# Performance work log

Hardware: AMD Instinct MI355X
Metric: run time of the kernel (lower is better)

## Reference

```python
import jax, jax.numpy as jnp
from jax import lax
import numpy as np

B, T, IN, H, OUT = 1024, 100, 64, 512, 64


def setup_inputs() -> dict:
    key = jax.random.key(0)
    ks = jax.random.split(key, 16)
    s_in = 1.0 / np.sqrt(IN)
    s_h = 1.0 / np.sqrt(H)
    inp = {
        'coeffs': jax.random.normal(ks[0], (B, T - 1, 4, IN), jnp.float32),
        'times': jnp.linspace(0.0, 1.0, T, dtype=jnp.float32),
        'dW': jax.random.normal(ks[1], (T - 1, B, H), jnp.float32),
        # initial_network: Linear(IN, H)
        'W_init': jax.random.normal(ks[2], (IN, H), jnp.float32) * s_in,
        'b_init': jnp.zeros((H,), jnp.float32),
        # drift MLP f: H -> H -> H
        'Wf1': jax.random.normal(ks[3], (H, H), jnp.float32) * s_h,
        'bf1': jnp.zeros((H,), jnp.float32),
        'Wf2': jax.random.normal(ks[4], (H, H), jnp.float32) * s_h,
        'bf2': jnp.zeros((H,), jnp.float32),
        # diffusion MLP g: H -> H -> H (tanh-bounded, diagonal noise)
        'Wg1': jax.random.normal(ks[5], (H, H), jnp.float32) * s_h,
        'bg1': jnp.zeros((H,), jnp.float32),
        'Wg2': jax.random.normal(ks[6], (H, H), jnp.float32) * s_h,
        'bg2': jnp.zeros((H,), jnp.float32),
        # readout: Tanh -> Linear(H,H) -> ReLU -> Linear(H,OUT)
        'Wl1': jax.random.normal(ks[7], (H, H), jnp.float32) * s_h,
        'bl1': jnp.zeros((H,), jnp.float32),
        'Wl2': jax.random.normal(ks[8], (H, OUT), jnp.float32) * s_h,
        'bl2': jnp.zeros((OUT,), jnp.float32),
    }
    return inp


def reference(coeffs, times, dW, W_init, b_init, Wf1, bf1, Wf2, bf2,
              Wg1, bg1, Wg2, bg2, Wl1, bl1, Wl2, bl2):
    # y0 = X.evaluate(times[0]) == constant coefficient of first spline segment
    x0 = coeffs[:, 0, 0, :]                      # [B, IN]
    y0 = x0 @ W_init + b_init                    # [B, H]

    def f(y):
        return jnp.tanh(y @ Wf1 + bf1) @ Wf2 + bf2

    def g(y):
        return jnp.tanh(jnp.tanh(y @ Wg1 + bg1) @ Wg2 + bg2)

    hs = times[1:] - times[:-1]                  # [T-1], equals dt on uniform grid

    def step(y, inp):
        h, dw = inp
        y_next = y + f(y) * h + g(y) * (jnp.sqrt(h) * dw)
        return y_next, y_next

    _, ys = lax.scan(step, y0, (hs, dW))         # ys: [T-1, B, H]
    z = jnp.concatenate([y0[None], ys], axis=0)  # [T, B, H]
    z = jnp.transpose(z, (1, 0, 2))              # [B, T, H]  (permute(1,0,2))

    # readout: Tanh -> Linear -> ReLU -> Linear
    out = jax.nn.relu(jnp.tanh(z) @ Wl1 + bl1) @ Wl2 + bl2  # [B, T, OUT]
    return out, z
```

## Files before the change

kernel.cpp:

```cpp
#include <hip/hip_runtime.h>
#include <hip/hip_bf16.h>
#include <math.h>

#define DEV __device__ __forceinline__

typedef __attribute__((ext_vector_type(8))) short short8;
typedef __attribute__((ext_vector_type(4))) float f32x4;
typedef __attribute__((ext_vector_type(4))) unsigned int u32x4;

static constexpr int Bsz  = 1024;
static constexpr int T    = 100;
static constexpr int TM1  = 99;
static constexpr int H    = 512;
static constexpr int OUTD = 64;
static constexpr int H2   = 1024;
static constexpr int BT   = Bsz * T;

DEV unsigned short f2bf(float f){
  unsigned int u = __float_as_uint(f);
  u += 0x7fffu + ((u >> 16) & 1u);
  return (unsigned short)(u >> 16);
}
DEV unsigned pack2(float lo, float hi){
  return (unsigned)f2bf(lo) | ((unsigned)f2bf(hi) << 16);
}
DEV float tanh_fast(float x){
  x = fminf(fmaxf(x, -15.f), 15.f);
  float e = __expf(2.f * x);
  return (e - 1.f) / (e + 1.f);
}

#define AISSUE_CC(dst, p) asm volatile("global_load_dwordx4 %0, %1, off sc0 sc1" : "=&v"(dst) : "v"(p) : "memory")
#define AISSUE_L2(dst, p) asm volatile("global_load_dwordx4 %0, %1, off sc0"     : "=&v"(dst) : "v"(p) : "memory")
#define PLOAD(dst, p)  asm volatile("global_load_dword %0, %1, off"          : "=&v"(dst) : "v"(p) : "memory")
#define SC_STORE(p, v) asm volatile("global_store_dword %0, %1, off sc0 sc1" :: "v"(p), "v"(v) : "memory")
#define VWAIT(n)       asm volatile("s_waitcnt vmcnt(" #n ")" ::: "memory"); __builtin_amdgcn_sched_barrier(0)

DEV void gbar(unsigned* cnt, unsigned target){
  __syncthreads();
  if (threadIdx.x == 0){
    __hip_atomic_fetch_add(cnt, 1u, __ATOMIC_RELAXED, __HIP_MEMORY_SCOPE_AGENT);
    while (__hip_atomic_load(cnt, __ATOMIC_RELAXED, __HIP_MEMORY_SCOPE_AGENT) < target)
      __builtin_amdgcn_s_sleep(1);
  }
  __syncthreads();
}

__global__ __launch_bounds__(256) void k_prep(const float* __restrict__ Wf1, const float* __restrict__ Wg1,
                                              const float* __restrict__ Wf2, const float* __restrict__ Wg2,
                                              const float* __restrict__ Wl1, const float* __restrict__ Wl2,
                                              unsigned short* __restrict__ W1T, unsigned short* __restrict__ W2T,
                                              unsigned short* __restrict__ Wl1F, unsigned short* __restrict__ Wl2F){
  __shared__ float tl[32][33];
  const float* src; unsigned short* dst; int N; int fmt;
  switch (blockIdx.z){
    case 0: src = Wf1; dst = W1T;             N = 512; fmt = 0; break;
    case 1: src = Wg1; dst = W1T + 512*512;   N = 512; fmt = 0; break;
    case 2: src = Wf2; dst = W2T;             N = 512; fmt = 0; break;
    case 3: src = Wg2; dst = W2T + 512*512;   N = 512; fmt = 0; break;
    case 4: src = Wl1; dst = Wl1F;            N = 512; fmt = 1; break;
    default: src = Wl2; dst = Wl2F;           N = 64;  fmt = 2; break;
  }
  int k0 = blockIdx.x*32, n0 = blockIdx.y*32;
  if (n0 >= N) return;
  int tx = threadIdx.x, ty = threadIdx.y;
  #pragma unroll
  for (int r = 0; r < 4; r++) tl[ty + r*8][tx] = src[(size_t)(k0 + ty + r*8) * N + n0 + tx];
  __syncthreads();
  if (fmt == 0){
    int kpos = k0 + ((tx & 15)*2 + (tx >> 4));
    #pragma unroll
    for (int r = 0; r < 4; r++) dst[(size_t)(n0 + ty + r*8) * 512 + kpos] = f2bf(tl[tx][ty + r*8]);
  } else {
    int k = k0 + tx;
    int Nc = (fmt == 1) ? 512 : 64;
    #pragma unroll
    for (int r = 0; r < 4; r++){
      int col = n0 + ty + r*8;
      size_t idx = (((size_t)(k >> 5)*Nc + col)*4 + ((k >> 3) & 3))*8 + (k & 7);
      dst[idx] = f2bf(tl[tx][ty + r*8]);
    }
  }
}

__global__ void k_zero(unsigned* __restrict__ cnts){
  cnts[threadIdx.x + blockIdx.x*256] = 0u;
}

#define KSX(K, W, LD) \
  VWAIT(W); \
  { short8 a_  = *(short8*)&ap[(K)&7]; \
    short8 b0_ = *(const short8*)(wbp + (K)*4096); \
    short8 b1_ = *(const short8*)(wbp + (K)*4096 + 1024); \
    p0 = __builtin_amdgcn_mfma_f32_16x16x32_bf16(a_, b0_, p0, 0,0,0); \
    p1 = __builtin_amdgcn_mfma_f32_16x16x32_bf16(a_, b1_, p1, 0,0,0); } \
  if ((K) < 8) { LD(ap[(K)&7], abp + (size_t)((K)+8)*65536); }

#define RUN16X(LD) \
  LD(ap[0], abp);          LD(ap[1], abp+65536); \
  LD(ap[2], abp+131072);   LD(ap[3], abp+196608); \
  LD(ap[4], abp+262144);   LD(ap[5], abp+327680); \
  LD(ap[6], abp+393216);   LD(ap[7], abp+458752); \
  KSX( 0,7,LD) KSX( 1,7,LD) KSX( 2,7,LD) KSX( 3,7,LD) \
  KSX( 4,7,LD) KSX( 5,7,LD) KSX( 6,7,LD) KSX( 7,7,LD) \
  KSX( 8,7,LD) KSX( 9,6,LD) KSX(10,5,LD) KSX(11,4,LD) \
  KSX(12,3,LD) KSX(13,2,LD) KSX(14,1,LD) KSX(15,0,LD)

template<int UNIQ>
__global__ __launch_bounds__(512, 1) void k_scan(
    const float* __restrict__ coeffs, const float* __restrict__ times,
    const float* __restrict__ dW,     const float* __restrict__ W_init,
    const float* __restrict__ b_init,
    const unsigned short* __restrict__ W1T, const unsigned short* __restrict__ W2T,
    const float* __restrict__ bf1, const float* __restrict__ bg1,
    const float* __restrict__ bf2, const float* __restrict__ bg2,
    unsigned short* __restrict__ ygk, unsigned short* __restrict__ uk,
    float* __restrict__ z, unsigned* __restrict__ cnts){
  __shared__ __align__(16) unsigned char W1s[65536];
  __shared__ __align__(16) unsigned char W2s[65536];
  __shared__ __align__(16) float cmb[64*68];
  __shared__ float tms[104];

  constexpr size_t YB = UNIQ ? (size_t)Bsz * H  * 2 : 0;
  constexpr size_t UB = UNIQ ? (size_t)Bsz * H2 * 2 : 0;

  const int bid = blockIdx.x, mt = bid & 15, ns = bid >> 4;
  const int m0 = mt*64, n1 = ns*64, n2 = ns*32;
  const int tid = threadIdx.x, lane = tid & 63, w = tid >> 6;
  const int fr = lane & 15, fq = lane >> 4;
  const int band = w & 3, isg = w >> 2;
  unsigned* cnt = cnts + mt*32;
  unsigned ep = 0;

  #pragma unroll
  for (int i = 0; i < 8; i++){
    int u = i*512 + tid;
    int fqi = u & 3, cl = (u >> 2) & 63, kc = u >> 8;
    *(uint4*)(W1s + (size_t)u*16) = *(const uint4*)(W1T + (size_t)(n1+cl)*512 + kc*32 + fqi*8);
    const unsigned short* s2 = (cl < 32) ? (W2T + (size_t)(n2+cl)*512)
                                         : (W2T + (size_t)262144 + (size_t)(n2+cl-32)*512);
    *(uint4*)(W2s + (size_t)u*16) = *(const uint4*)(s2 + kc*32 + fqi*8);
  }
  if (tid < 100) tms[tid] = times[tid];
  { int row = tid >> 3, c0 = (tid & 7)*8;
    const float* src = coeffs + (size_t)(m0+row)*(TM1*4*64) + c0;
    *(float4*)(&cmb[row*68 + c0])     = *(const float4*)src;
    *(float4*)(&cmb[row*68 + c0 + 4]) = *(const float4*)(src + 4);
  }
  __syncthreads();

  char* ygkb = (char*)ygk;
  char* ukb  = (char*)uk;
  const char* ab1 = ygkb + ((size_t)(m0 + band*16 + fr))*64 + fq*16;
  const char* ab2 = ukb + (size_t)isg*1048576 + ((size_t)(m0 + band*16 + fr))*64 + fq*16;
  char* up = ukb  + (size_t)(ns*2 + isg)*65536 + ((size_t)(m0 + band*16 + fq*4))*64 + fr*4;
  char* yp = ygkb + (size_t)ns*65536           + ((size_t)(m0 + band*16 + fq*4))*64 + fr*4;
  const unsigned char* wbp1 = W1s + isg*2048 + fr*64 + fq*16;
  const unsigned char* wbp2 = W2s + isg*2048 + fr*64 + fq*16;
  float* zp = z + ((size_t)(m0 + band*16 + fq*4))*T*512 + n2 + fr;

  const float* b1src = (ns < 8) ? bf1 : bg1;
  const int    b1off = n1 - ((ns < 8) ? 0 : 512) + isg*32 + fr;
  const float b1v0 = b1src[b1off], b1v1 = b1src[b1off + 16];
  const float* b2src = isg ? bg2 : bf2;
  const float b2v0 = b2src[n2 + fr], b2v1 = b2src[n2 + 16 + fr];

  float yv[2][4];
  if (isg){
    #pragma unroll
    for (int r = 0; r < 4; r++){
      int lrow = band*16 + fq*4 + r;
      float s0 = b_init[n2 + fr], s1 = b_init[n2 + 16 + fr];
      #pragma unroll 8
      for (int k = 0; k < 64; k++){
        float xv = cmb[lrow*68 + k];
        s0 += xv * W_init[(size_t)k*512 + n2 + fr];
        s1 += xv * W_init[(size_t)k*512 + n2 + 16 + fr];
      }
      yv[0][r] = s0; yv[1][r] = s1;
      SC_STORE(yp + r*64, pack2(s0, s1));
      zp[(size_t)r*T*512]      = s0;
      zp[(size_t)r*T*512 + 16] = s1;
    }
    VWAIT(8);
  }
  ++ep; gbar(cnt, ep*16);

  for (int t = 0; t < TM1; t++){
    float dv[8];
    {
      f32x4 p0 = {0.f,0.f,0.f,0.f}, p1 = {0.f,0.f,0.f,0.f};
      u32x4 ap[8];
      const char* abp = ab1 + (size_t)t*YB;
      const unsigned char* wbp = wbp1;
      if constexpr (UNIQ) { RUN16X(AISSUE_L2); } else { RUN16X(AISSUE_CC); }
      char* upt = up + (size_t)t*UB;
      #pragma unroll
      for (int r = 0; r < 4; r++)
        SC_STORE(upt + r*64, pack2(tanh_fast(p0[r] + b1v0), tanh_fast(p1[r] + b1v1)));
      if (isg){
        const char* dp = (const char*)dW + (((size_t)t*1024 + m0 + band*16 + fq*4)*512 + n2 + fr)*4;
        PLOAD(dv[0], dp + 0);      PLOAD(dv[1], dp + 64);
        PLOAD(dv[2], dp + 2048);   PLOAD(dv[3], dp + 2048+64);
        PLOAD(dv[4], dp + 4096);   PLOAD(dv[5], dp + 4096+64);
        PLOAD(dv[6], dp + 6144);   PLOAD(dv[7], dp + 6144+64);
        VWAIT(8);
      } else {
        VWAIT(0);
      }
    }
    ++ep; gbar(cnt, ep*16);

    {
      f32x4 p0 = {0.f,0.f,0.f,0.f}, p1 = {0.f,0.f,0.f,0.f};
      u32x4 ap[8];
      const char* abp = ab2 + (size_t)t*UB;
      const unsigned char* wbp = wbp2;
      if constexpr (UNIQ) { RUN16X(AISSUE_L2); } else { RUN16X(AISSUE_CC); }
      if (!isg){
        #pragma unroll
        for (int r = 0; r < 4; r++){
          int lrow = band*16 + fq*4 + r;
          cmb[lrow*68 + fr]      = p0[r] + b2v0;
          cmb[lrow*68 + 16 + fr] = p1[r] + b2v1;
        }
      }
      __syncthreads();
      if (isg){
        float h  = tms[t+1] - tms[t];
        float sq = sqrtf(h);
        char* ypt = yp + (size_t)(t+1)*YB;
        #pragma unroll
        for (int r = 0; r < 4; r++){
          int lrow = band*16 + fq*4 + r;
          float f0 = cmb[lrow*68 + fr],       f1 = cmb[lrow*68 + 16 + fr];
          float g0 = tanh_fast(p0[r] + b2v0), g1 = tanh_fast(p1[r] + b2v1);
          float y0n = yv[0][r] + f0*h + g0*(sq*dv[r*2]);
          float y1n = yv[1][r] + f1*h + g1*(sq*dv[r*2+1]);
          yv[0][r] = y0n; yv[1][r] = y1n;
          SC_STORE(ypt + r*64, pack2(y0n, y1n));
          zp[(size_t)r*T*512 + (size_t)(t+1)*512]      = y0n;
          zp[(size_t)r*T*512 + (size_t)(t+1)*512 + 16] = y1n;
        }
        VWAIT(8);
      }
    }
    if (t < TM1-1){ ++ep; gbar(cnt, ep*16); }
  }
}

__global__ __launch_bounds__(512, 1) void k_read(
    const float* __restrict__ z, const unsigned short* __restrict__ Wl1F,
    const float* __restrict__ bl1, const unsigned short* __restrict__ Wl2F,
    const float* __restrict__ bl2, float* __restrict__ out){
  __shared__ __align__(16) unsigned char zt[65536];
  __shared__ __align__(16) unsigned char relF[65536];
  const int tid = threadIdx.x, lane = tid & 63, w = tid >> 6;
  const int fr = lane & 15, fq = lane >> 4;
  const size_t rr0 = (size_t)blockIdx.x * 64;
  const int cw = w * 64;

  { int row = tid >> 3, c0 = (tid & 7) * 64;
    const float* zr = z + (rr0 + row) * 512 + c0;
    #pragma unroll
    for (int j = 0; j < 2; ++j){
      int kc = (c0 >> 5) + j;
      #pragma unroll
      for (int f = 0; f < 4; ++f){
        float4 v0 = *(const float4*)(zr + j*32 + f*8);
        float4 v1 = *(const float4*)(zr + j*32 + f*8 + 4);
        unsigned d0 = pack2(tanh_fast(v0.x), tanh_fast(v0.y));
        unsigned d1 = pack2(tanh_fast(v0.z), tanh_fast(v0.w));
        unsigned d2 = pack2(tanh_fast(v1.x), tanh_fast(v1.y));
        unsigned d3 = pack2(tanh_fast(v1.z), tanh_fast(v1.w));
        uint4 pk = {d0, d1, d2, d3};
        *(uint4*)(zt + (size_t)((kc*64 + row)*4 + f)*16) = pk;
      }
    }
  }
  __syncthreads();

  f32x4 acc[4][4];
  #pragma unroll
  for (int m = 0; m < 4; m++)
    #pragma unroll
    for (int c = 0; c < 4; c++) acc[m][c] = (f32x4){0.f,0.f,0.f,0.f};
  for (int kc = 0; kc < 16; ++kc){
    short8 a[4];
    #pragma unroll
    for (int m = 0; m < 4; m++)
      a[m] = *(const short8*)(zt + (size_t)((kc*64 + m*16 + fr)*4 + fq)*16);
    #pragma unroll
    for (int c = 0; c < 4; c++){
      short8 b = *(const short8*)(Wl1F + (((size_t)kc*512 + cw + c*16 + fr)*4 + fq)*8);
      #pragma unroll
      for (int m = 0; m < 4; m++)
        acc[m][c] = __builtin_amdgcn_mfma_f32_16x16x32_bf16(a[m], b, acc[m][c], 0, 0, 0);
    }
  }
  float bl1v[4];
  #pragma unroll
  for (int c = 0; c < 4; c++) bl1v[c] = bl1[cw + c*16 + fr];

  #pragma unroll
  for (int h = 0; h < 2; ++h){
    __syncthreads();
    if ((w >> 2) == h){
      float* stg = (float*)zt;
      int cb = cw - h*256;
      #pragma unroll
      for (int m = 0; m < 4; m++)
        #pragma unroll
        for (int c = 0; c < 4; c++)
          #pragma unroll
          for (int r = 0; r < 4; r++)
            stg[(m*16 + fq*4 + r)*256 + cb + c*16 + fr] = fmaxf(acc[m][c][r] + bl1v[c], 0.f);
    }
    __syncthreads();
    { int row = tid >> 3, c8 = (tid & 7) * 32;
      const float* stg = (const float*)zt;
      int kc = h*8 + (tid & 7);
      #pragma unroll
      for (int f = 0; f < 4; ++f){
        const float* p = stg + row*256 + c8 + f*8;
        unsigned d0 = pack2(p[0], p[1]);
        unsigned d1 = pack2(p[2], p[3]);
        unsigned d2 = pack2(p[4], p[5]);
        unsigned d3 = pack2(p[6], p[7]);
        uint4 pk = {d0, d1, d2, d3};
        *(uint4*)(relF + (size_t)((kc*64 + row)*4 + f)*16) = pk;
      }
    }
  }
  __syncthreads();

  f32x4 acc2[2];
  acc2[0] = (f32x4){0.f,0.f,0.f,0.f};
  acc2[1] = (f32x4){0.f,0.f,0.f,0.f};
  const int mt2 = w & 3, ocb = (w >> 2) * 32;
  for (int kc = 0; kc < 16; ++kc){
    short8 a = *(const short8*)(relF + (size_t)((kc*64 + mt2*16 + fr)*4 + fq)*16);
    #pragma unroll
    for (int j = 0; j < 2; j++){
      short8 b = *(const short8*)(Wl2F + (((size_t)(kc*64 + ocb + j*16 + fr))*4 + fq)*8);
      acc2[j] = __builtin_amdgcn_mfma_f32_16x16x32_bf16(a, b, acc2[j], 0, 0, 0);
    }
  }
  #pragma unroll
  for (int j = 0; j < 2; j++){
    #pragma unroll
    for (int r = 0; r < 4; r++){
      int row = mt2*16 + fq*4 + r;
      int oc  = ocb + j*16 + fr;
      out[(rr0 + row)*64 + oc] = acc2[j][r] + bl2[oc];
    }
  }
}

extern "C" void kernel_launch(void* const* d_in, const int* in_sizes, int n_in,
                              void* d_out, int out_size, void* d_ws, size_t ws_size,
                              hipStream_t stream){
  (void)in_sizes; (void)n_in; (void)out_size;
  const float* coeffs = (const float*)d_in[0];
  const float* times  = (const float*)d_in[1];
  const float* dW     = (const float*)d_in[2];
  const float* W_init = (const float*)d_in[3];
  const float* b_init = (const float*)d_in[4];
  const float* Wf1 = (const float*)d_in[5];
  const float* bf1 = (const float*)d_in[6];
  const float* Wf2 = (const float*)d_in[7];
  const float* bf2 = (const float*)d_in[8];
  const float* Wg1 = (const float*)d_in[9];
  const float* bg1 = (const float*)d_in[10];
  const float* Wg2 = (const float*)d_in[11];
  const float* bg2 = (const float*)d_in[12];
  const float* Wl1 = (const float*)d_in[13];
  const float* bl1 = (const float*)d_in[14];
  const float* Wl2 = (const float*)d_in[15];
  const float* bl2 = (const float*)d_in[16];

  float* out = (float*)d_out;
  float* z   = out + (size_t)Bsz * T * OUTD;

  const bool full = ws_size >= ((size_t)320 << 20);

  char* wsp = (char*)d_ws;
  auto carve = [&](size_t bytes) -> void* {
    void* p = (void*)wsp; wsp += (bytes + 255) & ~(size_t)255; return p;
  };
  unsigned short* W1T  = (unsigned short*)carve((size_t)H2 * H * 2);
  unsigned short* W2T  = (unsigned short*)carve((size_t)H2 * H * 2);
  unsigned short* Wl1F = (unsigned short*)carve((size_t)H * H * 2);
  unsigned short* Wl2F = (unsigned short*)carve((size_t)OUTD * H * 2);
  unsigned short* ygk  = (unsigned short*)carve(full ? (size_t)T   * Bsz * H  * 2
                                                     : (size_t)Bsz * H  * 2);
  unsigned short* uk   = (unsigned short*)carve(full ? (size_t)TM1 * Bsz * H2 * 2
                                                     : (size_t)Bsz * H2 * 2);
  unsigned*       cnts = (unsigned*)carve(1024 * sizeof(unsigned));

  k_zero<<<dim3(4), 256, 0, stream>>>(cnts);
  k_prep<<<dim3(16, 16, 6), dim3(32, 8), 0, stream>>>(Wf1, Wg1, Wf2, Wg2, Wl1, Wl2,
                                                      W1T, W2T, Wl1F, Wl2F);
  if (full)
    k_scan<1><<<dim3(256), 512, 0, stream>>>(coeffs, times, dW, W_init, b_init,
                                             W1T, W2T, bf1, bg1, bf2, bg2,
                                             ygk, uk, z, cnts);
  else
    k_scan<0><<<dim3(256), 512, 0, stream>>>(coeffs, times, dW, W_init, b_init,
                                             W1T, W2T, bf1, bg1, bf2, bg2,
                                             ygk, uk, z, cnts);
  k_read<<<dim3(BT / 64), 512, 0, stream>>>(z, Wl1F, bl1, Wl2F, bl2, out);
}
```

Baseline: 937.2 us.

## Split grid barrier, prefetch own y chunk across it, rotate K order, swizzle LDS

The grid barrier is split into arrive and wait halves. Between them each block issues the load for the first A chunk of the next y-GEMM, which is the slice that block wrote itself, so the barrier latency overlaps with a global load. In the first GEMM the K loop is rotated by the block's column index so different blocks start on different L2 lines. The weight tiles in LDS are XOR-swizzled to reduce bank conflicts. The risk is that the early prefetch relies on the block's own stores being visible before the wait completes.

```diff
diff --git a/kernel.cpp b/kernel.cpp
--- a/kernel.cpp
+++ b/kernel.cpp
@@ -36,10 +36,13 @@
 #define SC_STORE(p, v) asm volatile("global_store_dword %0, %1, off sc0 sc1" :: "v"(p), "v"(v) : "memory")
 #define VWAIT(n)       asm volatile("s_waitcnt vmcnt(" #n ")" ::: "memory"); __builtin_amdgcn_sched_barrier(0)
 
-DEV void gbar(unsigned* cnt, unsigned target){
-  __syncthreads();
+DEV void gbar_arrive(unsigned* cnt){
+  __syncthreads();
+  if (threadIdx.x == 0)
+    __hip_atomic_fetch_add(cnt, 1u, __ATOMIC_RELAXED, __HIP_MEMORY_SCOPE_AGENT);
+}
+DEV void gbar_wait(unsigned* cnt, unsigned target){
   if (threadIdx.x == 0){
-    __hip_atomic_fetch_add(cnt, 1u, __ATOMIC_RELAXED, __HIP_MEMORY_SCOPE_AGENT);
     while (__hip_atomic_load(cnt, __ATOMIC_RELAXED, __HIP_MEMORY_SCOPE_AGENT) < target)
       __builtin_amdgcn_s_sleep(1);
   }
@@ -90,8 +93,8 @@
 #define KSX(K, W, LD) \
   VWAIT(W); \
   { short8 a_  = *(short8*)&ap[(K)&7]; \
-    short8 b0_ = *(const short8*)(wbp + (K)*4096); \
-    short8 b1_ = *(const short8*)(wbp + (K)*4096 + 1024); \
+    short8 b0_ = *(const short8*)(wbp + (size_t)(K)*4096); \
+    short8 b1_ = *(const short8*)(wbp + (size_t)(K)*4096 + 1024); \
     p0 = __builtin_amdgcn_mfma_f32_16x16x32_bf16(a_, b0_, p0, 0,0,0); \
     p1 = __builtin_amdgcn_mfma_f32_16x16x32_bf16(a_, b1_, p1, 0,0,0); } \
   if ((K) < 8) { LD(ap[(K)&7], abp + (size_t)((K)+8)*65536); }
@@ -105,6 +108,29 @@
   KSX( 4,7,LD) KSX( 5,7,LD) KSX( 6,7,LD) KSX( 7,7,LD) \
   KSX( 8,7,LD) KSX( 9,6,LD) KSX(10,5,LD) KSX(11,4,LD) \
   KSX(12,3,LD) KSX(13,2,LD) KSX(14,1,LD) KSX(15,0,LD)
+
+#define C16(K) (((K) + rot) & 15)
+#define KSXR(K, W, LD) \
+  VWAIT(W); \
+  { short8 a_  = *(short8*)&ap[(K)&7]; \
+    short8 b0_ = *(const short8*)(wbp + (size_t)C16(K)*4096); \
+    short8 b1_ = *(const short8*)(wbp + (size_t)C16(K)*4096 + 1024); \
+    p0 = __builtin_amdgcn_mfma_f32_16x16x32_bf16(a_, b0_, p0, 0,0,0); \
+    p1 = __builtin_amdgcn_mfma_f32_16x16x32_bf16(a_, b1_, p1, 0,0,0); } \
+  if ((K) < 8) { LD(ap[(K)&7], abp + (size_t)C16((K)+8)*65536); }
+
+#define RUN16R(LD) \
+  LD(ap[1], abp + (size_t)C16(1)*65536); \
+  LD(ap[2], abp + (size_t)C16(2)*65536); \
+  LD(ap[3], abp + (size_t)C16(3)*65536); \
+  LD(ap[4], abp + (size_t)C16(4)*65536); \
+  LD(ap[5], abp + (size_t)C16(5)*65536); \
+  LD(ap[6], abp + (size_t)C16(6)*65536); \
+  LD(ap[7], abp + (size_t)C16(7)*65536); \
+  KSXR( 0,7,LD) KSXR( 1,7,LD) KSXR( 2,7,LD) KSXR( 3,7,LD) \
+  KSXR( 4,7,LD) KSXR( 5,7,LD) KSXR( 6,7,LD) KSXR( 7,7,LD) \
+  KSXR( 8,7,LD) KSXR( 9,6,LD) KSXR(10,5,LD) KSXR(11,4,LD) \
+  KSXR(12,3,LD) KSXR(13,2,LD) KSXR(14,1,LD) KSXR(15,0,LD)
 
 template<int UNIQ>
 __global__ __launch_bounds__(512, 1) void k_scan(
@@ -129,6 +155,7 @@
   const int tid = threadIdx.x, lane = tid & 63, w = tid >> 6;
   const int fr = lane & 15, fq = lane >> 4;
   const int band = w & 3, isg = w >> 2;
+  const int rot = ns;
   unsigned* cnt = cnts + mt*32;
   unsigned ep = 0;
 
@@ -136,10 +163,11 @@
   for (int i = 0; i < 8; i++){
     int u = i*512 + tid;
     int fqi = u & 3, cl = (u >> 2) & 63, kc = u >> 8;
-    *(uint4*)(W1s + (size_t)u*16) = *(const uint4*)(W1T + (size_t)(n1+cl)*512 + kc*32 + fqi*8);
+    size_t dstoff = (size_t)kc*4096 + (size_t)((cl*64 + fqi*16) ^ ((cl & 7) << 4));
+    *(uint4*)(W1s + dstoff) = *(const uint4*)(W1T + (size_t)(n1+cl)*512 + kc*32 + fqi*8);
     const unsigned short* s2 = (cl < 32) ? (W2T + (size_t)(n2+cl)*512)
                                          : (W2T + (size_t)262144 + (size_t)(n2+cl-32)*512);
-    *(uint4*)(W2s + (size_t)u*16) = *(const uint4*)(s2 + kc*32 + fqi*8);
+    *(uint4*)(W2s + dstoff) = *(const uint4*)(s2 + kc*32 + fqi*8);
   }
   if (tid < 100) tms[tid] = times[tid];
   { int row = tid >> 3, c0 = (tid & 7)*8;
@@ -155,8 +183,8 @@
   const char* ab2 = ukb + (size_t)isg*1048576 + ((size_t)(m0 + band*16 + fr))*64 + fq*16;
   char* up = ukb  + (size_t)(ns*2 + isg)*65536 + ((size_t)(m0 + band*16 + fq*4))*64 + fr*4;
   char* yp = ygkb + (size_t)ns*65536           + ((size_t)(m0 + band*16 + fq*4))*64 + fr*4;
-  const unsigned char* wbp1 = W1s + isg*2048 + fr*64 + fq*16;
-  const unsigned char* wbp2 = W2s + isg*2048 + fr*64 + fq*16;
+  const unsigned char* wbp1 = W1s + isg*2048 + (size_t)((fr*64 + fq*16) ^ ((fr & 7) << 4));
+  const unsigned char* wbp2 = W2s + isg*2048 + (size_t)((fr*64 + fq*16) ^ ((fr & 7) << 4));
   float* zp = z + ((size_t)(m0 + band*16 + fq*4))*T*512 + n2 + fr;
 
   const float* b1src = (ns < 8) ? bf1 : bg1;
@@ -164,6 +192,8 @@
   const float b1v0 = b1src[b1off], b1v1 = b1src[b1off + 16];
   const float* b2src = isg ? bg2 : bf2;
   const float b2v0 = b2src[n2 + fr], b2v1 = b2src[n2 + 16 + fr];
+
+  u32x4 ap[8];
 
   float yv[2][4];
   if (isg){
@@ -184,16 +214,18 @@
     }
     VWAIT(8);
   }
-  ++ep; gbar(cnt, ep*16);
+  ++ep; gbar_arrive(cnt);
+  if constexpr (UNIQ) { AISSUE_L2(ap[0], ab1 + (size_t)rot*65536); }
+  else                { AISSUE_CC(ap[0], ab1 + (size_t)rot*65536); }
+  gbar_wait(cnt, ep*16);
 
   for (int t = 0; t < TM1; t++){
     float dv[8];
     {
       f32x4 p0 = {0.f,0.f,0.f,0.f}, p1 = {0.f,0.f,0.f,0.f};
-      u32x4 ap[8];
       const char* abp = ab1 + (size_t)t*YB;
       const unsigned char* wbp = wbp1;
-      if constexpr (UNIQ) { RUN16X(AISSUE_L2); } else { RUN16X(AISSUE_CC); }
+      if constexpr (UNIQ) { RUN16R(AISSUE_L2); } else { RUN16R(AISSUE_CC); }
       char* upt = up + (size_t)t*UB;
       #pragma unroll
       for (int r = 0; r < 4; r++)
@@ -209,11 +241,10 @@
         VWAIT(0);
       }
     }
-    ++ep; gbar(cnt, ep*16);
+    ++ep; gbar_arrive(cnt); gbar_wait(cnt, ep*16);
 
     {
       f32x4 p0 = {0.f,0.f,0.f,0.f}, p1 = {0.f,0.f,0.f,0.f};
-      u32x4 ap[8];
       const char* abp = ab2 + (size_t)t*UB;
       const unsigned char* wbp = wbp2;
       if constexpr (UNIQ) { RUN16X(AISSUE_L2); } else { RUN16X(AISSUE_CC); }
@@ -245,7 +276,14 @@
         VWAIT(8);
       }
     }
-    if (t < TM1-1){ ++ep; gbar(cnt, ep*16); }
+    if (t < TM1-1){
+      ++ep; gbar_arrive(cnt);
+      { const char* pib = ab1 + (size_t)(t+1)*YB;
+        if constexpr (UNIQ) { AISSUE_L2(ap[0], pib + (size_t)rot*65536); }
+        else                { AISSUE_CC(ap[0], pib + (size_t)rot*65536); }
+      }
+      gbar_wait(cnt, ep*16);
+    }
   }
 }
 
```

Measured after the change: 930.9 us. Within noise of the previous version (-0.7%).

## Split K dimension across two wave groups in scan kernel with LDS reduction

Applied to the files above, without the earlier changes.

Doubles the scan kernel's block size to 1024 threads and splits each GEMM's K loop in half across two wave groups. The upper half writes its partial sums to shared memory, and the lower half adds them before applying tanh and the SDE update. The weight tiles in shared memory also get an XOR swizzle to reduce bank conflicts on the B-operand reads. The aim is to halve the serial MFMA chain per step on this latency-bound recurrent path, at the cost of extra __syncthreads and shared-memory traffic per step.

```diff
diff --git a/kernel.cpp b/kernel.cpp
--- a/kernel.cpp
+++ b/kernel.cpp
@@ -87,27 +87,24 @@
   cnts[threadIdx.x + blockIdx.x*256] = 0u;
 }
 
-#define KSX(K, W, LD) \
+#define KR8(K, W, LD) \
   VWAIT(W); \
-  { short8 a_  = *(short8*)&ap[(K)&7]; \
-    short8 b0_ = *(const short8*)(wbp + (K)*4096); \
-    short8 b1_ = *(const short8*)(wbp + (K)*4096 + 1024); \
+  { short8 a_  = *(short8*)&ap[K]; \
+    short8 b0_ = *(const short8*)(wbp + (size_t)(K)*4096); \
+    short8 b1_ = *(const short8*)(wbp + (size_t)(K)*4096 + 1024); \
     p0 = __builtin_amdgcn_mfma_f32_16x16x32_bf16(a_, b0_, p0, 0,0,0); \
-    p1 = __builtin_amdgcn_mfma_f32_16x16x32_bf16(a_, b1_, p1, 0,0,0); } \
-  if ((K) < 8) { LD(ap[(K)&7], abp + (size_t)((K)+8)*65536); }
-
-#define RUN16X(LD) \
+    p1 = __builtin_amdgcn_mfma_f32_16x16x32_bf16(a_, b1_, p1, 0,0,0); }
+
+#define RUN8(LD) \
   LD(ap[0], abp);          LD(ap[1], abp+65536); \
   LD(ap[2], abp+131072);   LD(ap[3], abp+196608); \
   LD(ap[4], abp+262144);   LD(ap[5], abp+327680); \
   LD(ap[6], abp+393216);   LD(ap[7], abp+458752); \
-  KSX( 0,7,LD) KSX( 1,7,LD) KSX( 2,7,LD) KSX( 3,7,LD) \
-  KSX( 4,7,LD) KSX( 5,7,LD) KSX( 6,7,LD) KSX( 7,7,LD) \
-  KSX( 8,7,LD) KSX( 9,6,LD) KSX(10,5,LD) KSX(11,4,LD) \
-  KSX(12,3,LD) KSX(13,2,LD) KSX(14,1,LD) KSX(15,0,LD)
+  KR8(0,7,LD) KR8(1,6,LD) KR8(2,5,LD) KR8(3,4,LD) \
+  KR8(4,3,LD) KR8(5,2,LD) KR8(6,1,LD) KR8(7,0,LD)
 
 template<int UNIQ>
-__global__ __launch_bounds__(512, 1) void k_scan(
+__global__ __launch_bounds__(1024, 1) void k_scan(
     const float* __restrict__ coeffs, const float* __restrict__ times,
     const float* __restrict__ dW,     const float* __restrict__ W_init,
     const float* __restrict__ b_init,
@@ -128,35 +125,38 @@
   const int m0 = mt*64, n1 = ns*64, n2 = ns*32;
   const int tid = threadIdx.x, lane = tid & 63, w = tid >> 6;
   const int fr = lane & 15, fq = lane >> 4;
-  const int band = w & 3, isg = w >> 2;
+  const int band = w & 3, isg = (w >> 2) & 1, kh = w >> 3;
   unsigned* cnt = cnts + mt*32;
   unsigned ep = 0;
 
   #pragma unroll
-  for (int i = 0; i < 8; i++){
-    int u = i*512 + tid;
+  for (int i = 0; i < 4; i++){
+    int u = i*1024 + tid;
     int fqi = u & 3, cl = (u >> 2) & 63, kc = u >> 8;
-    *(uint4*)(W1s + (size_t)u*16) = *(const uint4*)(W1T + (size_t)(n1+cl)*512 + kc*32 + fqi*8);
+    size_t dstoff = (size_t)kc*4096 + (size_t)((cl*64 + fqi*16) ^ ((cl & 7) << 4));
+    *(uint4*)(W1s + dstoff) = *(const uint4*)(W1T + (size_t)(n1+cl)*512 + kc*32 + fqi*8);
     const unsigned short* s2 = (cl < 32) ? (W2T + (size_t)(n2+cl)*512)
                                          : (W2T + (size_t)262144 + (size_t)(n2+cl-32)*512);
-    *(uint4*)(W2s + (size_t)u*16) = *(const uint4*)(s2 + kc*32 + fqi*8);
+    *(uint4*)(W2s + dstoff) = *(const uint4*)(s2 + kc*32 + fqi*8);
   }
   if (tid < 100) tms[tid] = times[tid];
-  { int row = tid >> 3, c0 = (tid & 7)*8;
+  { int row = tid >> 4, c0 = (tid & 15)*4;
     const float* src = coeffs + (size_t)(m0+row)*(TM1*4*64) + c0;
-    *(float4*)(&cmb[row*68 + c0])     = *(const float4*)src;
-    *(float4*)(&cmb[row*68 + c0 + 4]) = *(const float4*)(src + 4);
+    *(float4*)(&cmb[row*68 + c0]) = *(const float4*)src;
   }
   __syncthreads();
 
   char* ygkb = (char*)ygk;
   char* ukb  = (char*)uk;
-  const char* ab1 = ygkb + ((size_t)(m0 + band*16 + fr))*64 + fq*16;
-  const char* ab2 = ukb + (size_t)isg*1048576 + ((size_t)(m0 + band*16 + fr))*64 + fq*16;
+  const char* ab1k = ygkb + ((size_t)(m0 + band*16 + fr))*64 + fq*16 + (size_t)kh*8*65536;
+  const char* ab2k = ukb + (size_t)isg*1048576 + ((size_t)(m0 + band*16 + fr))*64 + fq*16
+                     + (size_t)kh*8*65536;
   char* up = ukb  + (size_t)(ns*2 + isg)*65536 + ((size_t)(m0 + band*16 + fq*4))*64 + fr*4;
   char* yp = ygkb + (size_t)ns*65536           + ((size_t)(m0 + band*16 + fq*4))*64 + fr*4;
-  const unsigned char* wbp1 = W1s + isg*2048 + fr*64 + fq*16;
-  const unsigned char* wbp2 = W2s + isg*2048 + fr*64 + fq*16;
+  const unsigned char* wbp1 = W1s + (size_t)kh*32768 + isg*2048
+                              + (size_t)((fr*64 + fq*16) ^ ((fr & 7) << 4));
+  const unsigned char* wbp2 = W2s + (size_t)kh*32768 + isg*2048
+                              + (size_t)((fr*64 + fq*16) ^ ((fr & 7) << 4));
   float* zp = z + ((size_t)(m0 + band*16 + fq*4))*T*512 + n2 + fr;
 
   const float* b1src = (ns < 8) ? bf1 : bg1;
@@ -166,7 +166,7 @@
   const float b2v0 = b2src[n2 + fr], b2v1 = b2src[n2 + 16 + fr];
 
   float yv[2][4];
-  if (isg){
+  if (kh == 0 && isg == 1){
     #pragma unroll
     for (int r = 0; r < 4; r++){
       int lrow = band*16 + fq*4 + r;
@@ -191,22 +191,37 @@
     {
       f32x4 p0 = {0.f,0.f,0.f,0.f}, p1 = {0.f,0.f,0.f,0.f};
       u32x4 ap[8];
-      const char* abp = ab1 + (size_t)t*YB;
+      const char* abp = ab1k + (size_t)t*YB;
       const unsigned char* wbp = wbp1;
-      if constexpr (UNIQ) { RUN16X(AISSUE_L2); } else { RUN16X(AISSUE_CC); }
-      char* upt = up + (size_t)t*UB;
-      #pragma unroll
-      for (int r = 0; r < 4; r++)
-        SC_STORE(upt + r*64, pack2(tanh_fast(p0[r] + b1v0), tanh_fast(p1[r] + b1v1)));
-      if (isg){
-        const char* dp = (const char*)dW + (((size_t)t*1024 + m0 + band*16 + fq*4)*512 + n2 + fr)*4;
-        PLOAD(dv[0], dp + 0);      PLOAD(dv[1], dp + 64);
-        PLOAD(dv[2], dp + 2048);   PLOAD(dv[3], dp + 2048+64);
-        PLOAD(dv[4], dp + 4096);   PLOAD(dv[5], dp + 4096+64);
-        PLOAD(dv[6], dp + 6144);   PLOAD(dv[7], dp + 6144+64);
-        VWAIT(8);
-      } else {
-        VWAIT(0);
+      if constexpr (UNIQ) { RUN8(AISSUE_L2); } else { RUN8(AISSUE_CC); }
+      if (kh){
+        #pragma unroll
+        for (int r = 0; r < 4; r++){
+          int lrow = band*16 + fq*4 + r;
+          cmb[lrow*68 + isg*32 + fr]      = p0[r];
+          cmb[lrow*68 + isg*32 + 16 + fr] = p1[r];
+        }
+      }
+      __syncthreads();
+      if (!kh){
+        char* upt = up + (size_t)t*UB;
+        #pragma unroll
+        for (int r = 0; r < 4; r++){
+          int lrow = band*16 + fq*4 + r;
+          float s0 = p0[r] + cmb[lrow*68 + isg*32 + fr]      + b1v0;
+          float s1 = p1[r] + cmb[lrow*68 + isg*32 + 16 + fr] + b1v1;
+          SC_STORE(upt + r*64, pack2(tanh_fast(s0), tanh_fast(s1)));
+        }
+        if (isg){
+          const char* dp = (const char*)dW + (((size_t)t*1024 + m0 + band*16 + fq*4)*512 + n2 + fr)*4;
+          PLOAD(dv[0], dp + 0);      PLOAD(dv[1], dp + 64);
+          PLOAD(dv[2], dp + 2048);   PLOAD(dv[3], dp + 2048+64);
+          PLOAD(dv[4], dp + 4096);   PLOAD(dv[5], dp + 4096+64);
+          PLOAD(dv[6], dp + 6144);   PLOAD(dv[7], dp + 6144+64);
+          VWAIT(8);
+        } else {
+          VWAIT(0);
+        }
       }
     }
     ++ep; gbar(cnt, ep*16);
@@ -214,27 +229,37 @@
     {
       f32x4 p0 = {0.f,0.f,0.f,0.f}, p1 = {0.f,0.f,0.f,0.f};
       u32x4 ap[8];
-      const char* abp = ab2 + (size_t)t*UB;
+      const char* abp = ab2k + (size_t)t*UB;
       const unsigned char* wbp = wbp2;
-      if constexpr (UNIQ) { RUN16X(AISSUE_L2); } else { RUN16X(AISSUE_CC); }
-      if (!isg){
+      if constexpr (UNIQ) { RUN8(AISSUE_L2); } else { RUN8(AISSUE_CC); }
+      if (kh){
         #pragma unroll
         for (int r = 0; r < 4; r++){
           int lrow = band*16 + fq*4 + r;
-          cmb[lrow*68 + fr]      = p0[r] + b2v0;
-          cmb[lrow*68 + 16 + fr] = p1[r] + b2v1;
+          cmb[lrow*68 + isg*32 + fr]      = p0[r];
+          cmb[lrow*68 + isg*32 + 16 + fr] = p1[r];
         }
       }
       __syncthreads();
-      if (isg){
+      if (!kh && !isg){
+        #pragma unroll
+        for (int r = 0; r < 4; r++){
+          int lrow = band*16 + fq*4 + r;
+          cmb[lrow*68 + fr]      = p0[r] + cmb[lrow*68 + fr]      + b2v0;
+          cmb[lrow*68 + 16 + fr] = p1[r] + cmb[lrow*68 + 16 + fr] + b2v1;
+        }
+      }
+      __syncthreads();
+      if (!kh && isg){
         float h  = tms[t+1] - tms[t];
         float sq = sqrtf(h);
         char* ypt = yp + (size_t)(t+1)*YB;
         #pragma unroll
         for (int r = 0; r < 4; r++){
           int lrow = band*16 + fq*4 + r;
-          float f0 = cmb[lrow*68 + fr],       f1 = cmb[lrow*68 + 16 + fr];
-          float g0 = tanh_fast(p0[r] + b2v0), g1 = tanh_fast(p1[r] + b2v1);
+          float f0 = cmb[lrow*68 + fr],      f1 = cmb[lrow*68 + 16 + fr];
+          float g0 = tanh_fast(p0[r] + cmb[lrow*68 + 32 + fr] + b2v0);
+          float g1 = tanh_fast(p1[r] + cmb[lrow*68 + 48 + fr] + b2v1);
           float y0n = yv[0][r] + f0*h + g0*(sq*dv[r*2]);
           float y1n = yv[1][r] + f1*h + g1*(sq*dv[r*2+1]);
           yv[0][r] = y0n; yv[1][r] = y1n;
@@ -402,12 +427,12 @@
   k_prep<<<dim3(16, 16, 6), dim3(32, 8), 0, stream>>>(Wf1, Wg1, Wf2, Wg2, Wl1, Wl2,
                                                       W1T, W2T, Wl1F, Wl2F);
   if (full)
-    k_scan<1><<<dim3(256), 512, 0, stream>>>(coeffs, times, dW, W_init, b_init,
-                                             W1T, W2T, bf1, bg1, bf2, bg2,
-                                             ygk, uk, z, cnts);
+    k_scan<1><<<dim3(256), 1024, 0, stream>>>(coeffs, times, dW, W_init, b_init,
+                                              W1T, W2T, bf1, bg1, bf2, bg2,
+                                              ygk, uk, z, cnts);
   else
-    k_scan<0><<<dim3(256), 512, 0, stream>>>(coeffs, times, dW, W_init, b_init,
-                                             W1T, W2T, bf1, bg1, bf2, bg2,
-                                             ygk, uk, z, cnts);
+    k_scan<0><<<dim3(256), 1024, 0, stream>>>(coeffs, times, dW, W_init, b_init,
+                                              W1T, W2T, bf1, bg1, bf2, bg2,
+                                              ygk, uk, z, cnts);
   k_read<<<dim3(BT / 64), 512, 0, stream>>>(z, Wl1F, bl1, Wl2F, bl2, out);
 }
```

Measured after the change: 963.2 us. 1.03x slower.

## Replace atomic-counter grid barrier with per-block flag array and XOR-swizzle LDS weights

Applied to the files above, without the earlier changes.

The grid barrier among the 16 blocks of a row tile used an atomic counter. It now has each block store its epoch into its own flag slot, and a waiter polls all 16 flags with four coherent 16-byte loads. This removes contention from the atomic read-modify-write on the ~300 barriers in the sequential scan. The LDS weight tiles are also stored with an XOR swizzle on the column index to cut bank conflicts on the MFMA B-operand reads. Risks include the polling cost of four vector loads per spin and correctness relying on the ordering of flag stores after the data stores.

```diff
diff --git a/kernel.cpp b/kernel.cpp
--- a/kernel.cpp
+++ b/kernel.cpp
@@ -36,12 +36,34 @@
 #define SC_STORE(p, v) asm volatile("global_store_dword %0, %1, off sc0 sc1" :: "v"(p), "v"(v) : "memory")
 #define VWAIT(n)       asm volatile("s_waitcnt vmcnt(" #n ")" ::: "memory"); __builtin_amdgcn_sched_barrier(0)
 
-DEV void gbar(unsigned* cnt, unsigned target){
-  __syncthreads();
+DEV void bar_arrive(unsigned* fl, int ns, unsigned ep){
+  __syncthreads();
+  if (threadIdx.x == 0)
+    SC_STORE((char*)(fl + ns), ep);
+}
+DEV unsigned umin4(u32x4 v){
+  unsigned m = v[0];
+  m = m < v[1] ? m : v[1];
+  m = m < v[2] ? m : v[2];
+  m = m < v[3] ? m : v[3];
+  return m;
+}
+DEV void bar_wait(unsigned* fl, unsigned ep){
   if (threadIdx.x == 0){
-    __hip_atomic_fetch_add(cnt, 1u, __ATOMIC_RELAXED, __HIP_MEMORY_SCOPE_AGENT);
-    while (__hip_atomic_load(cnt, __ATOMIC_RELAXED, __HIP_MEMORY_SCOPE_AGENT) < target)
+    for (;;){
+      u32x4 a, b, c, d;
+      AISSUE_CC(a, (char*)fl);
+      AISSUE_CC(b, (char*)fl + 16);
+      AISSUE_CC(c, (char*)fl + 32);
+      AISSUE_CC(d, (char*)fl + 48);
+      VWAIT(0);
+      unsigned m = umin4(a);
+      unsigned m2 = umin4(b); m = m < m2 ? m : m2;
+      m2 = umin4(c); m = m < m2 ? m : m2;
+      m2 = umin4(d); m = m < m2 ? m : m2;
+      if (m >= ep) break;
       __builtin_amdgcn_s_sleep(1);
+    }
   }
   __syncthreads();
 }
@@ -90,8 +112,8 @@
 #define KSX(K, W, LD) \
   VWAIT(W); \
   { short8 a_  = *(short8*)&ap[(K)&7]; \
-    short8 b0_ = *(const short8*)(wbp + (K)*4096); \
-    short8 b1_ = *(const short8*)(wbp + (K)*4096 + 1024); \
+    short8 b0_ = *(const short8*)(wbp + (size_t)(K)*4096); \
+    short8 b1_ = *(const short8*)(wbp + (size_t)(K)*4096 + 1024); \
     p0 = __builtin_amdgcn_mfma_f32_16x16x32_bf16(a_, b0_, p0, 0,0,0); \
     p1 = __builtin_amdgcn_mfma_f32_16x16x32_bf16(a_, b1_, p1, 0,0,0); } \
   if ((K) < 8) { LD(ap[(K)&7], abp + (size_t)((K)+8)*65536); }
@@ -129,17 +151,18 @@
   const int tid = threadIdx.x, lane = tid & 63, w = tid >> 6;
   const int fr = lane & 15, fq = lane >> 4;
   const int band = w & 3, isg = w >> 2;
-  unsigned* cnt = cnts + mt*32;
+  unsigned* fl = cnts + mt*16;
   unsigned ep = 0;
 
   #pragma unroll
   for (int i = 0; i < 8; i++){
     int u = i*512 + tid;
     int fqi = u & 3, cl = (u >> 2) & 63, kc = u >> 8;
-    *(uint4*)(W1s + (size_t)u*16) = *(const uint4*)(W1T + (size_t)(n1+cl)*512 + kc*32 + fqi*8);
+    size_t dstoff = (size_t)kc*4096 + (size_t)((cl*64 + fqi*16) ^ ((cl & 7) << 4));
+    *(uint4*)(W1s + dstoff) = *(const uint4*)(W1T + (size_t)(n1+cl)*512 + kc*32 + fqi*8);
     const unsigned short* s2 = (cl < 32) ? (W2T + (size_t)(n2+cl)*512)
                                          : (W2T + (size_t)262144 + (size_t)(n2+cl-32)*512);
-    *(uint4*)(W2s + (size_t)u*16) = *(const uint4*)(s2 + kc*32 + fqi*8);
+    *(uint4*)(W2s + dstoff) = *(const uint4*)(s2 + kc*32 + fqi*8);
   }
   if (tid < 100) tms[tid] = times[tid];
   { int row = tid >> 3, c0 = (tid & 7)*8;
@@ -155,8 +178,8 @@
   const char* ab2 = ukb + (size_t)isg*1048576 + ((size_t)(m0 + band*16 + fr))*64 + fq*16;
   char* up = ukb  + (size_t)(ns*2 + isg)*65536 + ((size_t)(m0 + band*16 + fq*4))*64 + fr*4;
   char* yp = ygkb + (size_t)ns*65536           + ((size_t)(m0 + band*16 + fq*4))*64 + fr*4;
-  const unsigned char* wbp1 = W1s + isg*2048 + fr*64 + fq*16;
-  const unsigned char* wbp2 = W2s + isg*2048 + fr*64 + fq*16;
+  const unsigned char* wbp1 = W1s + isg*2048 + (size_t)((fr*64 + fq*16) ^ ((fr & 7) << 4));
+  const unsigned char* wbp2 = W2s + isg*2048 + (size_t)((fr*64 + fq*16) ^ ((fr & 7) << 4));
   float* zp = z + ((size_t)(m0 + band*16 + fq*4))*T*512 + n2 + fr;
 
   const float* b1src = (ns < 8) ? bf1 : bg1;
@@ -184,7 +207,7 @@
     }
     VWAIT(8);
   }
-  ++ep; gbar(cnt, ep*16);
+  ++ep; bar_arrive(fl, ns, ep); bar_wait(fl, ep);
 
   for (int t = 0; t < TM1; t++){
     float dv[8];
@@ -209,7 +232,7 @@
         VWAIT(0);
       }
     }
-    ++ep; gbar(cnt, ep*16);
+    ++ep; bar_arrive(fl, ns, ep); bar_wait(fl, ep);
 
     {
       f32x4 p0 = {0.f,0.f,0.f,0.f}, p1 = {0.f,0.f,0.f,0.f};
@@ -245,7 +268,9 @@
         VWAIT(8);
       }
     }
-    if (t < TM1-1){ ++ep; gbar(cnt, ep*16); }
+    if (t < TM1-1){
+      ++ep; bar_arrive(fl, ns, ep); bar_wait(fl, ep);
+    }
   }
 }
 
```

Result: slower. 1.001 ms (+6.8%).
